# Kernel optimization log

Measured on AMD Instinct MI355X. Metric: run time of the kernel, lower is better.

The kernel has to match this reference:

```python
import jax, jax.numpy as jnp
from jax import lax
import numpy as np

# Problem dims (see init_kwargs)
B, CIN, H, W = 4, 128, 128, 128
COUT, K, STRIDE, PAD, DIL, GROUPS, OG = 128, 3, 1, 1, 1, 1, 2


def setup_inputs() -> dict:
    key = jax.random.key(0)
    k0, k1, k2 = jax.random.split(key, 3)
    x = jax.random.normal(k0, (B, CIN, H, W), dtype=jnp.float32)
    off_ch = 3 * OG * K * K  # with_mask=True -> scale=3 (dy, dx, mask)
    # Small random offset-conv weights so offsets are non-trivial (zero-init would degenerate to plain conv)
    w_off = jax.random.normal(k1, (off_ch, CIN, K, K), dtype=jnp.float32) * 0.01
    b_off = jnp.zeros((off_ch,), jnp.float32)
    stdv = 1.0 / np.sqrt(CIN * K * K)
    weight = jax.random.uniform(k2, (COUT, CIN // GROUPS, K, K), jnp.float32, -stdv, stdv)
    bias = jnp.zeros((COUT,), jnp.float32)
    return {"x": x, "w_off": w_off, "b_off": b_off, "weight": weight, "bias": bias}


def _deform_conv2d(x, offset, mask, weight, bias):
    # x: [B,C,H,W]; offset: [B,2*OG*K2,Ho,Wo]; mask: [B,OG*K2,Ho,Wo]
    Bn, C, Hn, Wn = x.shape
    O = weight.shape[0]
    K2 = K * K
    Ho = (Hn + 2 * PAD - DIL * (K - 1) - 1) // STRIDE + 1
    Wo = (Wn + 2 * PAD - DIL * (K - 1) - 1) // STRIDE + 1
    # torchvision layout: per offset group, per kernel point, (dy, dx) interleaved
    off = offset.reshape(Bn, OG, K2, 2, Ho, Wo)
    kg = (jnp.arange(K) * DIL).astype(x.dtype)
    kyf = jnp.repeat(kg, K)  # [K2] kernel row offset, k2 = i*K + j
    kxf = jnp.tile(kg, K)    # [K2] kernel col offset
    base_y = (jnp.arange(Ho) * STRIDE - PAD).astype(x.dtype)
    base_x = (jnp.arange(Wo) * STRIDE - PAD).astype(x.dtype)
    # sampling coords: [B,OG,K2,Ho,Wo]
    sy = base_y[None, None, None, :, None] + kyf[None, None, :, None, None] + off[:, :, :, 0]
    sx = base_x[None, None, None, None, :] + kxf[None, None, :, None, None] + off[:, :, :, 1]
    y0f = jnp.floor(sy)
    x0f = jnp.floor(sx)
    ly = sy - y0f  # bilinear fractional weights
    lx = sx - x0f
    y0 = y0f.astype(jnp.int32)
    x0 = x0f.astype(jnp.int32)
    Cg = C // OG
    xg = x.reshape(Bn, OG, Cg, Hn * Wn)

    def gather(iy, ix):
        # zero-padding semantics: out-of-range corners contribute 0
        valid = ((iy >= 0) & (iy < Hn) & (ix >= 0) & (ix < Wn)).astype(x.dtype)
        idx = (jnp.clip(iy, 0, Hn - 1) * Wn + jnp.clip(ix, 0, Wn - 1)).reshape(Bn, OG, 1, -1)
        v = jnp.take_along_axis(xg, idx, axis=3).reshape(Bn, OG, Cg, K2, Ho, Wo)
        return v * valid[:, :, None]

    v00 = gather(y0, x0)
    v01 = gather(y0, x0 + 1)
    v10 = gather(y0 + 1, x0)
    v11 = gather(y0 + 1, x0 + 1)
    wy = ly[:, :, None]  # broadcast over channel dim
    wx = lx[:, :, None]
    val = (v00 * (1 - wy) * (1 - wx) + v01 * (1 - wy) * wx
           + v10 * wy * (1 - wx) + v11 * wy * wx)
    # modulated DCNv2: multiply sampled values by sigmoid mask
    val = val * mask.reshape(Bn, OG, 1, K2, Ho, Wo)
    # im2col GEMM: cols [B,G,(C/G)*K2,Ho*Wo] x weight [G,O/G,(C/G)*K2]
    cols = val.reshape(Bn, GROUPS, (C // GROUPS) * K2, Ho * Wo)
    wg = weight.reshape(GROUPS, O // GROUPS, (C // GROUPS) * K2)
    out = jnp.einsum('gok,bgkn->bgon', wg, cols).reshape(Bn, O, Ho, Wo)
    return out + bias[None, :, None, None]


def reference(x, w_off, b_off, weight, bias):
    off_out = lax.conv_general_dilated(
        x, w_off, (STRIDE, STRIDE), [(PAD, PAD), (PAD, PAD)],
        rhs_dilation=(DIL, DIL), dimension_numbers=('NCHW', 'OIHW', 'NCHW')
    ) + b_off[None, :, None, None]
    oh, ow, m = jnp.split(off_out, 3, axis=1)
    offset = jnp.concatenate([oh, ow], axis=1)
    mask = jax.nn.sigmoid(m)
    return _deform_conv2d(x, offset, mask, weight, bias)
```

## Files before the change

kernel.cpp:

```cpp
#include <hip/hip_runtime.h>
#include <math.h>

#define NB 4
#define NC 128
#define NH 128
#define NW 128
#define NHW (NH*NW)
#define NCOUT 128

#define SY_OFF 0
#define SX_OFF 1179648
#define MK_OFF 2359296
#define WOFF_OFF 3538944
#define WMAIN_OFF 3580416
#define XT_OFF 3663360

typedef short short8 __attribute__((ext_vector_type(8)));
typedef float f32x4 __attribute__((ext_vector_type(4)));

__device__ inline short f2bf(float f) {
    unsigned u = __float_as_uint(f);
    u = (u + 0x7FFFu + ((u >> 16) & 1u)) >> 16;
    return (short)u;
}
__device__ inline unsigned pack2(float lo, float hi) {
    unsigned r;
    asm("v_cvt_pk_bf16_f32 %0, %1, %2" : "=v"(r) : "v"(lo), "v"(hi));
    return r;
}
__device__ inline float bflo(unsigned u) { return __uint_as_float(u << 16); }
__device__ inline float bfhi(unsigned u) { return __uint_as_float(u & 0xffff0000u); }
__device__ inline unsigned pkf16(float a, float b) {
    auto h = __builtin_amdgcn_cvt_pkrtz(a, b);
    unsigned r; __builtin_memcpy(&r, &h, 4); return r;
}
__device__ inline float f16f(unsigned s) {
    unsigned short us = (unsigned short)s;
    __fp16 h; __builtin_memcpy(&h, &us, 2); return (float)h;
}
__device__ inline void gload_lds16(const void* g, void* l) {
    __builtin_amdgcn_global_load_lds(
        (const __attribute__((address_space(1))) unsigned int*)g,
        (__attribute__((address_space(3))) unsigned int*)l, 16, 0, 0);
}

__global__ void wtrans_kernel(const float* __restrict__ w_off,
                              const float* __restrict__ weight,
                              float* __restrict__ ws)
{
    int i = blockIdx.x * 256 + threadIdx.x;
    if (i < 36*2304) {
        int s = i / 2304, rem = i - s*2304;
        int row = rem / 36, c = rem - row*36;
        int chunk = s / 9, k2 = s - 9*chunk;
        float v = (row < 54 && c < 32) ? w_off[(row*NC + chunk*32 + c)*9 + k2] : 0.f;
        ((short*)(ws + WOFF_OFF))[i] = f2bf(v);
    } else if (i < 36*2304 + 36*4608) {
        int j = i - 36*2304;
        int s = j / 4608, rem = j - s*4608;
        int row = rem / 36, c = rem - row*36;
        int chunk = s / 9, k2 = s - 9*chunk;
        float v = (c < 32) ? weight[(row*NC + chunk*32 + c)*9 + k2] : 0.f;
        ((short*)(ws + WMAIN_OFF))[j] = f2bf(v);
    }
}

__global__ __launch_bounds__(256) void xtrans_kernel(
    const float* __restrict__ x, float* __restrict__ ws)
{
    short* xT = (short*)(ws + XT_OFF);
    const int bid = blockIdx.x;
    const int ys = bid & 15, cg = (bid >> 4) & 15, b = bid >> 8;
    const int col = threadIdx.x & 127, rr = threadIdx.x >> 7;
    const float* xb = x + ((long)(b*NC + cg*8))*NHW;
#pragma unroll
    for (int yy = 0; yy < 4; ++yy) {
        const int y = ys*8 + yy*2 + rr;
        const float* p = xb + y*NW + col;
        float v[8];
#pragma unroll
        for (int q = 0; q < 8; ++q) v[q] = p[q*NHW];
        uint4 u = make_uint4(pack2(v[0],v[1]), pack2(v[2],v[3]),
                             pack2(v[4],v[5]), pack2(v[6],v[7]));
        *(uint4*)&xT[(((long)(b*16+cg)*NH + y)*NW + col)*8] = u;
    }
}

__global__ __launch_bounds__(512, 4) void offconv_kernel(
    float* __restrict__ ws, const float* __restrict__ b_off)
{
    __shared__ short wslab[2][2304];
    int bid = blockIdx.x;
    bid = (bid & 7) * 64 + (bid >> 3);
    const int b   = bid >> 7;
    const int ho  = bid & 127;
    const int tid = threadIdx.x;
    const int lane = tid & 63;
    const int wid = tid >> 6;
    const int n = lane & 15, g = lane >> 4;
    const int px = wid*16 + n;
    const short* woff = (const short*)(ws + WOFF_OFF);
    const char*  xTb  = (const char*)((const short*)(ws + XT_OFF) + (long)b*16*NHW*8);

    f32x4 acc[4];
#pragma unroll
    for (int rf = 0; rf < 4; ++rf) acc[rf] = (f32x4){0.f,0.f,0.f,0.f};

    auto DMA = [&](int it, int buf) {
        if (tid < 288) gload_lds16(woff + it*2304 + tid*8, &wslab[buf][tid*8]);
    };
    auto LOADB = [&](int it) -> short8 {
        const int chunk = it/9, k2 = it - 9*chunk;
        const int y = ho + k2/3 - 1, xc = px + (k2%3) - 1;
        short8 bf = (short8){0,0,0,0,0,0,0,0};
        if ((unsigned)y < NH && (unsigned)xc < NW)
            bf = *(const short8*)(xTb + ((long)(chunk*4 + g)*NHW + y*NW + xc)*16);
        return bf;
    };

    DMA(0, 0);
    short8 bcur = LOADB(0);
    __syncthreads();

#pragma unroll 1
    for (int it = 0; it < 36; ++it) {
        const int cur = it & 1, nxt = cur ^ 1;
        short8 bnext;
        if (it < 35) { DMA(it+1, nxt); bnext = LOADB(it+1); }
        __builtin_amdgcn_sched_barrier(0);
#pragma unroll
        for (int rf = 0; rf < 4; ++rf) {
            short8 af = *(const short8*)&wslab[cur][(rf*16 + n)*36 + 8*g];
            acc[rf] = __builtin_amdgcn_mfma_f32_16x16x32_bf16(af, bcur, acc[rf], 0,0,0);
        }
        __syncthreads();
        bcur = bnext;
    }

#pragma unroll
    for (int rf = 0; rf < 4; ++rf) {
#pragma unroll
        for (int r = 0; r < 4; ++r) {
            int cout = 16*rf + 4*g + r;
            if (cout >= 54) continue;
            float v = acc[rf][r] + b_off[cout];
            if (cout < 36) {
                int og = cout / 18, rem = cout - 18*og;
                int k2c = rem >> 1, d = cout & 1;
                float base = d ? (float)(px - 1 + (k2c % 3))
                              : (float)(ho - 1 + (k2c / 3));
                ws[(d ? SX_OFF : SY_OFF) + (((b*2+og)*9 + k2c)*NHW) + ho*NW + px] = v + base;
            } else {
                int cc = cout - 36;
                int og = cc / 9, k2c = cc - 9*og;
                ws[MK_OFF + (((b*2+og)*9 + k2c)*NHW) + ho*NW + px] = 1.f/(1.f+expf(-v));
            }
        }
    }
}

__global__ __launch_bounds__(512, 4) void deform_kernel(
    const float* __restrict__ ws_c, float* __restrict__ ws,
    const float* __restrict__ bias, float* __restrict__ out)
{
    __shared__ short4 pI[18][128];
    __shared__ uint2  pWp[18][128];
    __shared__ short  vals[2][128][40];
    __shared__ short  wslab[2][4608];

    int bid = blockIdx.x;
    bid = (bid & 7) * 64 + (bid >> 3);
    const int b   = bid >> 7;
    const int ho  = bid & 127;
    const int tid = threadIdx.x;
    const int lane = tid & 63;
    const int wid = tid >> 6;
    const int n = lane & 15, g = lane >> 4;
    const int ch  = wid & 1;
    const int pxq = wid >> 1;
    const int sp  = tid & 127;
    const int sub = tid >> 7;
    const short* wmn = (const short*)(ws + WMAIN_OFF);
    const char*  xTb = (const char*)((const short*)(ws + XT_OFF) + (long)b*16*NHW*8);

    f32x4 acc[4][2];
#pragma unroll
    for (int rf = 0; rf < 4; ++rf) {
        acc[rf][0] = (f32x4){0.f,0.f,0.f,0.f};
        acc[rf][1] = (f32x4){0.f,0.f,0.f,0.f};
    }

    auto DMA = [&](int slabIdx, int buf) {
        const short* src = wmn + slabIdx*4608;
        gload_lds16(src + tid*8, &wslab[buf][tid*8]);
        if (tid < 64) gload_lds16(src + 4096 + tid*8, &wslab[buf][4096 + tid*8]);
    };
    auto GLOAD = [&](int j, uint4* G) {
        const int chunk = j/9;
        const int row = (j/18)*9 + (j%9);
        const short4 I = pI[row][sp];
        const char* xp = xTb + (long)(chunk*4 + sub)*(NHW*16);
        G[0] = *(const uint4*)(xp + (((int)I.x) << 4));
        G[1] = *(const uint4*)(xp + (((int)I.y) << 4));
        G[2] = *(const uint4*)(xp + (((int)I.z) << 4));
        G[3] = *(const uint4*)(xp + (((int)I.w) << 4));
    };
    auto FIN = [&](int j, uint4* G, int buf) {
        const int row = (j/18)*9 + (j%9);
        const uint2 wp = *(const uint2*)&pWp[row][sp];
        const float W0 = f16f(wp.x), W1 = f16f(wp.x >> 16);
        const float W2 = f16f(wp.y), W3 = f16f(wp.y >> 16);
        uint4 u; unsigned* up = (unsigned*)&u;
        const unsigned* a = (const unsigned*)&G[0];
        const unsigned* bq = (const unsigned*)&G[1];
        const unsigned* c = (const unsigned*)&G[2];
        const unsigned* d = (const unsigned*)&G[3];
#pragma unroll
        for (int e = 0; e < 4; ++e) {
            float lo = W0*bflo(a[e]) + W1*bflo(bq[e]) + W2*bflo(c[e]) + W3*bflo(d[e]);
            float hi = W0*bfhi(a[e]) + W1*bfhi(bq[e]) + W2*bfhi(c[e]) + W3*bfhi(d[e]);
            up[e] = pack2(lo, hi);
        }
        *(uint4*)&vals[buf][sp][sub*8] = u;
    };

    DMA(0, 0);

    for (int e = tid; e < 2304; e += 512) {
        const int og = e / 1152, rem = e - og*1152;
        const int k2 = rem >> 7, px = rem & 127;
        const int sidx = (((b*2+og)*9 + k2)*NHW) + ho*NW + px;
        const float sy = ws[SY_OFF + sidx];
        const float sx = ws[SX_OFF + sidx];
        const float m  = ws[MK_OFF + sidx];
        const float y0f = floorf(sy), x0f = floorf(sx);
        const float ly = sy - y0f, lx = sx - x0f;
        const int y0 = (int)y0f, x0i = (int)x0f;
        const int y1 = y0 + 1, x1 = x0i + 1;
        const bool vy0 = (unsigned)y0 < NH, vy1 = (unsigned)y1 < NH;
        const bool vx0 = (unsigned)x0i < NW, vx1 = (unsigned)x1 < NW;
        const int cy0 = min(max(y0,0),NH-1), cy1 = min(max(y1,0),NH-1);
        const int cx0 = min(max(x0i,0),NW-1), cx1 = min(max(x1,0),NW-1);
        pI[og*9+k2][px] = make_short4(
            (short)(cy0*NW + cx0), (short)(cy0*NW + cx1),
            (short)(cy1*NW + cx0), (short)(cy1*NW + cx1));
        const float W0 = (vy0 && vx0) ? (1.f-ly)*(1.f-lx)*m : 0.f;
        const float W1 = (vy0 && vx1) ? (1.f-ly)*lx*m       : 0.f;
        const float W2 = (vy1 && vx0) ? ly*(1.f-lx)*m       : 0.f;
        const float W3 = (vy1 && vx1) ? ly*lx*m             : 0.f;
        pWp[og*9+k2][px] = make_uint2(pkf16(W0, W1), pkf16(W2, W3));
    }
    __syncthreads();

    uint4 GA[4], GB[4];
    GLOAD(0, GA);
    FIN(0, GA, 0);
    GLOAD(1, GB);
    asm volatile("s_waitcnt lgkmcnt(0)" ::: "memory");
    __builtin_amdgcn_s_barrier();
    __builtin_amdgcn_sched_barrier(0);

    auto BODY = [&](int it, uint4* Gfree, uint4* Gheld) {
        const int cur = it & 1, nxt = cur ^ 1;
        if (it < 35) DMA(it+1, nxt);
        if (it < 34) GLOAD(it+2, Gfree);
        __builtin_amdgcn_sched_barrier(0);
        {
            short8 bf0 = *(const short8*)&vals[cur][pxq*32 + n][8*g];
            short8 bf1 = *(const short8*)&vals[cur][pxq*32 + 16 + n][8*g];
#pragma unroll
            for (int rf = 0; rf < 4; ++rf) {
                short8 af = *(const short8*)&wslab[cur][(ch*64 + rf*16 + n)*36 + 8*g];
                acc[rf][0] = __builtin_amdgcn_mfma_f32_16x16x32_bf16(af, bf0, acc[rf][0], 0,0,0);
                acc[rf][1] = __builtin_amdgcn_mfma_f32_16x16x32_bf16(af, bf1, acc[rf][1], 0,0,0);
            }
        }
        __builtin_amdgcn_sched_barrier(0);
        if (it < 35) FIN(it+1, Gheld, nxt);
        if (it < 34) {
            asm volatile("s_waitcnt vmcnt(4) lgkmcnt(0)" ::: "memory");
            __builtin_amdgcn_s_barrier();
            __builtin_amdgcn_sched_barrier(0);
        } else if (it == 34) {
            asm volatile("s_waitcnt vmcnt(0) lgkmcnt(0)" ::: "memory");
            __builtin_amdgcn_s_barrier();
            __builtin_amdgcn_sched_barrier(0);
        }
    };
#pragma unroll 1
    for (int t = 0; t < 18; ++t) {
        BODY(2*t,     GA, GB);
        BODY(2*t + 1, GB, GA);
    }

#pragma unroll
    for (int rf = 0; rf < 4; ++rf) {
#pragma unroll
        for (int pxb = 0; pxb < 2; ++pxb) {
            const int px = pxq*32 + pxb*16 + n;
#pragma unroll
            for (int r = 0; r < 4; ++r) {
                const int cout = ch*64 + rf*16 + 4*g + r;
                out[((b*NCOUT + cout)*NH + ho)*NW + px] = acc[rf][pxb][r] + bias[cout];
            }
        }
    }
}

extern "C" void kernel_launch(void* const* d_in, const int* in_sizes, int n_in,
                              void* d_out, int out_size, void* d_ws, size_t ws_size,
                              hipStream_t stream)
{
    const float* x      = (const float*)d_in[0];
    const float* w_off  = (const float*)d_in[1];
    const float* b_off  = (const float*)d_in[2];
    const float* weight = (const float*)d_in[3];
    const float* bias   = (const float*)d_in[4];
    float* out = (float*)d_out;
    float* ws  = (float*)d_ws;

    hipLaunchKernelGGL(wtrans_kernel, dim3(972), dim3(256), 0, stream,
                       w_off, weight, ws);
    hipLaunchKernelGGL(xtrans_kernel, dim3(1024), dim3(256), 0, stream,
                       x, ws);
    hipLaunchKernelGGL(offconv_kernel, dim3(NB*NH), dim3(512), 0, stream,
                       ws, b_off);
    hipLaunchKernelGGL(deform_kernel, dim3(NB*NH), dim3(512), 0, stream,
                       ws, ws, bias, out);
}
```

Baseline: 92.58 us.

## Fuse offset conv into deformable conv kernel via shared-memory handoff

Merges the offset-convolution kernel and the deformable-conv kernel into one launch. Each block computes its row's offset/mask conv outputs into LDS and builds its bilinear sample tables from there, instead of writing sy/sx/mask planes to global workspace and reading them back. LDS regions are aliased so the combined kernel keeps a similar footprint. One scheduling barrier inside the main loop is also dropped. The cost is a longer per-block serial phase before the main GEMM pipeline starts, with less overlap across blocks.

```diff
diff --git a/kernel.cpp b/kernel.cpp
--- a/kernel.cpp
+++ b/kernel.cpp
@@ -8,9 +8,6 @@
 #define NHW (NH*NW)
 #define NCOUT 128
 
-#define SY_OFF 0
-#define SX_OFF 1179648
-#define MK_OFF 2359296
 #define WOFF_OFF 3538944
 #define WMAIN_OFF 3580416
 #define XT_OFF 3663360
@@ -86,10 +83,19 @@
     }
 }
 
-__global__ __launch_bounds__(512, 4) void offconv_kernel(
-    float* __restrict__ ws, const float* __restrict__ b_off)
+__global__ __launch_bounds__(512, 4) void fused_kernel(
+    const float* __restrict__ b_off, const float* __restrict__ bias,
+    float* __restrict__ ws, float* __restrict__ out)
 {
-    __shared__ short wslab[2][2304];
+    __shared__ short4 pI[18][128];
+    __shared__ uint2  pWp[18][128];
+    __shared__ char   creg[38912];
+
+    float* convout = (float*)creg;
+    short (*wsoff)[2304] = (short(*)[2304])(creg + 28512);
+    short (*vals)[128][40] = (short(*)[128][40])creg;
+    short (*wslab)[4608] = (short(*)[4608])(creg + 20480);
+
     int bid = blockIdx.x;
     bid = (bid & 7) * 64 + (bid >> 3);
     const int b   = bid >> 7;
@@ -98,90 +104,88 @@
     const int lane = tid & 63;
     const int wid = tid >> 6;
     const int n = lane & 15, g = lane >> 4;
-    const int px = wid*16 + n;
-    const short* woff = (const short*)(ws + WOFF_OFF);
-    const char*  xTb  = (const char*)((const short*)(ws + XT_OFF) + (long)b*16*NHW*8);
-
-    f32x4 acc[4];
-#pragma unroll
-    for (int rf = 0; rf < 4; ++rf) acc[rf] = (f32x4){0.f,0.f,0.f,0.f};
-
-    auto DMA = [&](int it, int buf) {
-        if (tid < 288) gload_lds16(woff + it*2304 + tid*8, &wslab[buf][tid*8]);
-    };
-    auto LOADB = [&](int it) -> short8 {
-        const int chunk = it/9, k2 = it - 9*chunk;
-        const int y = ho + k2/3 - 1, xc = px + (k2%3) - 1;
-        short8 bf = (short8){0,0,0,0,0,0,0,0};
-        if ((unsigned)y < NH && (unsigned)xc < NW)
-            bf = *(const short8*)(xTb + ((long)(chunk*4 + g)*NHW + y*NW + xc)*16);
-        return bf;
-    };
-
-    DMA(0, 0);
-    short8 bcur = LOADB(0);
-    __syncthreads();
-
-#pragma unroll 1
-    for (int it = 0; it < 36; ++it) {
-        const int cur = it & 1, nxt = cur ^ 1;
-        short8 bnext;
-        if (it < 35) { DMA(it+1, nxt); bnext = LOADB(it+1); }
-        __builtin_amdgcn_sched_barrier(0);
-#pragma unroll
-        for (int rf = 0; rf < 4; ++rf) {
-            short8 af = *(const short8*)&wslab[cur][(rf*16 + n)*36 + 8*g];
-            acc[rf] = __builtin_amdgcn_mfma_f32_16x16x32_bf16(af, bcur, acc[rf], 0,0,0);
-        }
-        __syncthreads();
-        bcur = bnext;
-    }
-
-#pragma unroll
-    for (int rf = 0; rf < 4; ++rf) {
-#pragma unroll
-        for (int r = 0; r < 4; ++r) {
-            int cout = 16*rf + 4*g + r;
-            if (cout >= 54) continue;
-            float v = acc[rf][r] + b_off[cout];
-            if (cout < 36) {
-                int og = cout / 18, rem = cout - 18*og;
-                int k2c = rem >> 1, d = cout & 1;
-                float base = d ? (float)(px - 1 + (k2c % 3))
-                              : (float)(ho - 1 + (k2c / 3));
-                ws[(d ? SX_OFF : SY_OFF) + (((b*2+og)*9 + k2c)*NHW) + ho*NW + px] = v + base;
-            } else {
-                int cc = cout - 36;
-                int og = cc / 9, k2c = cc - 9*og;
-                ws[MK_OFF + (((b*2+og)*9 + k2c)*NHW) + ho*NW + px] = 1.f/(1.f+expf(-v));
-            }
-        }
-    }
-}
-
-__global__ __launch_bounds__(512, 4) void deform_kernel(
-    const float* __restrict__ ws_c, float* __restrict__ ws,
-    const float* __restrict__ bias, float* __restrict__ out)
-{
-    __shared__ short4 pI[18][128];
-    __shared__ uint2  pWp[18][128];
-    __shared__ short  vals[2][128][40];
-    __shared__ short  wslab[2][4608];
-
-    int bid = blockIdx.x;
-    bid = (bid & 7) * 64 + (bid >> 3);
-    const int b   = bid >> 7;
-    const int ho  = bid & 127;
-    const int tid = threadIdx.x;
-    const int lane = tid & 63;
-    const int wid = tid >> 6;
-    const int n = lane & 15, g = lane >> 4;
+    const int px1 = wid*16 + n;
     const int ch  = wid & 1;
     const int pxq = wid >> 1;
     const int sp  = tid & 127;
     const int sub = tid >> 7;
-    const short* wmn = (const short*)(ws + WMAIN_OFF);
-    const char*  xTb = (const char*)((const short*)(ws + XT_OFF) + (long)b*16*NHW*8);
+    const short* woff = (const short*)(ws + WOFF_OFF);
+    const short* wmn  = (const short*)(ws + WMAIN_OFF);
+    const char*  xTb  = (const char*)((const short*)(ws + XT_OFF) + (long)b*16*NHW*8);
+
+    {
+        f32x4 accO[4];
+#pragma unroll
+        for (int rf = 0; rf < 4; ++rf) accO[rf] = (f32x4){0.f,0.f,0.f,0.f};
+
+        auto DMAo = [&](int it, int buf) {
+            if (tid < 288) gload_lds16(woff + it*2304 + tid*8, &wsoff[buf][tid*8]);
+        };
+        auto LOADB = [&](int it) -> short8 {
+            const int chunk = it/9, k2 = it - 9*chunk;
+            const int y = ho + k2/3 - 1, xc = px1 + (k2%3) - 1;
+            short8 bf = (short8){0,0,0,0,0,0,0,0};
+            if ((unsigned)y < NH && (unsigned)xc < NW)
+                bf = *(const short8*)(xTb + ((long)(chunk*4 + g)*NHW + y*NW + xc)*16);
+            return bf;
+        };
+
+        DMAo(0, 0);
+        short8 bcur = LOADB(0);
+        __syncthreads();
+
+#pragma unroll 1
+        for (int it = 0; it < 36; ++it) {
+            const int cur = it & 1, nxt = cur ^ 1;
+            short8 bnext;
+            if (it < 35) { DMAo(it+1, nxt); bnext = LOADB(it+1); }
+            __builtin_amdgcn_sched_barrier(0);
+#pragma unroll
+            for (int rf = 0; rf < 4; ++rf) {
+                short8 af = *(const short8*)&wsoff[cur][(rf*16 + n)*36 + 8*g];
+                accO[rf] = __builtin_amdgcn_mfma_f32_16x16x32_bf16(af, bcur, accO[rf], 0,0,0);
+            }
+            __syncthreads();
+            bcur = bnext;
+        }
+
+#pragma unroll
+        for (int rf = 0; rf < 4; ++rf) {
+#pragma unroll
+            for (int r = 0; r < 4; ++r) {
+                const int cout = 16*rf + 4*g + r;
+                if (cout < 54) convout[cout*132 + px1] = accO[rf][r];
+            }
+        }
+    }
+    __syncthreads();
+
+    for (int e = tid; e < 2304; e += 512) {
+        const int og = e / 1152, rem = e - og*1152;
+        const int k2 = rem >> 7, px = rem & 127;
+        const int c_sy = og*18 + 2*k2, c_sx = c_sy + 1, c_m = 36 + og*9 + k2;
+        const float sy = convout[c_sy*132 + px] + b_off[c_sy] + (float)(ho - 1 + k2/3);
+        const float sx = convout[c_sx*132 + px] + b_off[c_sx] + (float)(px - 1 + k2%3);
+        const float mr = convout[c_m*132 + px] + b_off[c_m];
+        const float m  = 1.f / (1.f + expf(-mr));
+        const float y0f = floorf(sy), x0f = floorf(sx);
+        const float ly = sy - y0f, lx = sx - x0f;
+        const int y0 = (int)y0f, x0i = (int)x0f;
+        const int y1 = y0 + 1, x1 = x0i + 1;
+        const bool vy0 = (unsigned)y0 < NH, vy1 = (unsigned)y1 < NH;
+        const bool vx0 = (unsigned)x0i < NW, vx1 = (unsigned)x1 < NW;
+        const int cy0 = min(max(y0,0),NH-1), cy1 = min(max(y1,0),NH-1);
+        const int cx0 = min(max(x0i,0),NW-1), cx1 = min(max(x1,0),NW-1);
+        pI[og*9+k2][px] = make_short4(
+            (short)(cy0*NW + cx0), (short)(cy0*NW + cx1),
+            (short)(cy1*NW + cx0), (short)(cy1*NW + cx1));
+        const float W0 = (vy0 && vx0) ? (1.f-ly)*(1.f-lx)*m : 0.f;
+        const float W1 = (vy0 && vx1) ? (1.f-ly)*lx*m       : 0.f;
+        const float W2 = (vy1 && vx0) ? ly*(1.f-lx)*m       : 0.f;
+        const float W3 = (vy1 && vx1) ? ly*lx*m             : 0.f;
+        pWp[og*9+k2][px] = make_uint2(pkf16(W0, W1), pkf16(W2, W3));
+    }
+    __syncthreads();
 
     f32x4 acc[4][2];
 #pragma unroll
@@ -190,7 +194,7 @@
         acc[rf][1] = (f32x4){0.f,0.f,0.f,0.f};
     }
 
-    auto DMA = [&](int slabIdx, int buf) {
+    auto DMAm = [&](int slabIdx, int buf) {
         const short* src = wmn + slabIdx*4608;
         gload_lds16(src + tid*8, &wslab[buf][tid*8]);
         if (tid < 64) gload_lds16(src + 4096 + tid*8, &wslab[buf][4096 + tid*8]);
@@ -224,35 +228,8 @@
         *(uint4*)&vals[buf][sp][sub*8] = u;
     };
 
-    DMA(0, 0);
-
-    for (int e = tid; e < 2304; e += 512) {
-        const int og = e / 1152, rem = e - og*1152;
-        const int k2 = rem >> 7, px = rem & 127;
-        const int sidx = (((b*2+og)*9 + k2)*NHW) + ho*NW + px;
-        const float sy = ws[SY_OFF + sidx];
-        const float sx = ws[SX_OFF + sidx];
-        const float m  = ws[MK_OFF + sidx];
-        const float y0f = floorf(sy), x0f = floorf(sx);
-        const float ly = sy - y0f, lx = sx - x0f;
-        const int y0 = (int)y0f, x0i = (int)x0f;
-        const int y1 = y0 + 1, x1 = x0i + 1;
-        const bool vy0 = (unsigned)y0 < NH, vy1 = (unsigned)y1 < NH;
-        const bool vx0 = (unsigned)x0i < NW, vx1 = (unsigned)x1 < NW;
-        const int cy0 = min(max(y0,0),NH-1), cy1 = min(max(y1,0),NH-1);
-        const int cx0 = min(max(x0i,0),NW-1), cx1 = min(max(x1,0),NW-1);
-        pI[og*9+k2][px] = make_short4(
-            (short)(cy0*NW + cx0), (short)(cy0*NW + cx1),
-            (short)(cy1*NW + cx0), (short)(cy1*NW + cx1));
-        const float W0 = (vy0 && vx0) ? (1.f-ly)*(1.f-lx)*m : 0.f;
-        const float W1 = (vy0 && vx1) ? (1.f-ly)*lx*m       : 0.f;
-        const float W2 = (vy1 && vx0) ? ly*(1.f-lx)*m       : 0.f;
-        const float W3 = (vy1 && vx1) ? ly*lx*m             : 0.f;
-        pWp[og*9+k2][px] = make_uint2(pkf16(W0, W1), pkf16(W2, W3));
-    }
-    __syncthreads();
-
     uint4 GA[4], GB[4];
+    DMAm(0, 0);
     GLOAD(0, GA);
     FIN(0, GA, 0);
     GLOAD(1, GB);
@@ -262,7 +239,7 @@
 
     auto BODY = [&](int it, uint4* Gfree, uint4* Gheld) {
         const int cur = it & 1, nxt = cur ^ 1;
-        if (it < 35) DMA(it+1, nxt);
+        if (it < 35) DMAm(it+1, nxt);
         if (it < 34) GLOAD(it+2, Gfree);
         __builtin_amdgcn_sched_barrier(0);
         {
@@ -275,7 +252,6 @@
                 acc[rf][1] = __builtin_amdgcn_mfma_f32_16x16x32_bf16(af, bf1, acc[rf][1], 0,0,0);
             }
         }
-        __builtin_amdgcn_sched_barrier(0);
         if (it < 35) FIN(it+1, Gheld, nxt);
         if (it < 34) {
             asm volatile("s_waitcnt vmcnt(4) lgkmcnt(0)" ::: "memory");
@@ -323,8 +299,6 @@
                        w_off, weight, ws);
     hipLaunchKernelGGL(xtrans_kernel, dim3(1024), dim3(256), 0, stream,
                        x, ws);
-    hipLaunchKernelGGL(offconv_kernel, dim3(NB*NH), dim3(512), 0, stream,
-                       ws, b_off);
-    hipLaunchKernelGGL(deform_kernel, dim3(NB*NH), dim3(512), 0, stream,
-                       ws, ws, bias, out);
-}
+    hipLaunchKernelGGL(fused_kernel, dim3(NB*NH), dim3(512), 0, stream,
+                       b_off, bias, ws, out);
+}
```

Measured after the change: 177.0 us. +91.1%, slower.

## Keep sampled columns in registers as MFMA A operand, split rows into half-row blocks

Applied to the files above, without the earlier changes.

The deformable conv kernel now launches twice as many 256-thread blocks, each covering half an output row (64 pixels). Each wave samples its own 16 pixels across 32 channels and feeds the bilinear result straight into the MFMA A operand from registers. This drops the vals LDS staging buffer and its write/read traffic. Each wave computes all 128 output channels, so weight slabs are read from LDS by every wave, and the output is written as float4 stores. The trade-off is more per-block setup and weight DMA per output pixel, in exchange for less LDS use and no intermediate LDS round trip.

```diff
diff --git a/kernel.cpp b/kernel.cpp
--- a/kernel.cpp
+++ b/kernel.cpp
@@ -159,77 +159,76 @@
     }
 }
 
-__global__ __launch_bounds__(512, 4) void deform_kernel(
+__global__ __launch_bounds__(256, 4) void deform_kernel(
     const float* __restrict__ ws_c, float* __restrict__ ws,
     const float* __restrict__ bias, float* __restrict__ out)
 {
-    __shared__ short4 pI[18][128];
-    __shared__ uint2  pWp[18][128];
-    __shared__ short  vals[2][128][40];
+    __shared__ short4 pI[18][64];
+    __shared__ uint2  pWp[18][64];
     __shared__ short  wslab[2][4608];
 
     int bid = blockIdx.x;
-    bid = (bid & 7) * 64 + (bid >> 3);
-    const int b   = bid >> 7;
-    const int ho  = bid & 127;
+    bid = (bid & 7) * 128 + (bid >> 3);
+    const int b   = bid >> 8;
+    const int ho  = (bid >> 1) & 127;
+    const int wb  = (bid & 1) * 64;
     const int tid = threadIdx.x;
     const int lane = tid & 63;
     const int wid = tid >> 6;
     const int n = lane & 15, g = lane >> 4;
-    const int ch  = wid & 1;
-    const int pxq = wid >> 1;
-    const int sp  = tid & 127;
-    const int sub = tid >> 7;
+    const int pxl = 16*wid + n;
     const short* wmn = (const short*)(ws + WMAIN_OFF);
     const char*  xTb = (const char*)((const short*)(ws + XT_OFF) + (long)b*16*NHW*8);
 
-    f32x4 acc[4][2];
-#pragma unroll
-    for (int rf = 0; rf < 4; ++rf) {
-        acc[rf][0] = (f32x4){0.f,0.f,0.f,0.f};
-        acc[rf][1] = (f32x4){0.f,0.f,0.f,0.f};
-    }
+    f32x4 acc[8];
+#pragma unroll
+    for (int rf = 0; rf < 8; ++rf) acc[rf] = (f32x4){0.f,0.f,0.f,0.f};
 
     auto DMA = [&](int slabIdx, int buf) {
         const short* src = wmn + slabIdx*4608;
         gload_lds16(src + tid*8, &wslab[buf][tid*8]);
+        gload_lds16(src + 2048 + tid*8, &wslab[buf][2048 + tid*8]);
         if (tid < 64) gload_lds16(src + 4096 + tid*8, &wslab[buf][4096 + tid*8]);
     };
-    auto GLOAD = [&](int j, uint4* G) {
-        const int chunk = j/9;
-        const int row = (j/18)*9 + (j%9);
-        const short4 I = pI[row][sp];
-        const char* xp = xTb + (long)(chunk*4 + sub)*(NHW*16);
-        G[0] = *(const uint4*)(xp + (((int)I.x) << 4));
-        G[1] = *(const uint4*)(xp + (((int)I.y) << 4));
-        G[2] = *(const uint4*)(xp + (((int)I.z) << 4));
-        G[3] = *(const uint4*)(xp + (((int)I.w) << 4));
-    };
-    auto FIN = [&](int j, uint4* G, int buf) {
-        const int row = (j/18)*9 + (j%9);
-        const uint2 wp = *(const uint2*)&pWp[row][sp];
-        const float W0 = f16f(wp.x), W1 = f16f(wp.x >> 16);
-        const float W2 = f16f(wp.y), W3 = f16f(wp.y >> 16);
-        uint4 u; unsigned* up = (unsigned*)&u;
-        const unsigned* a = (const unsigned*)&G[0];
-        const unsigned* bq = (const unsigned*)&G[1];
-        const unsigned* c = (const unsigned*)&G[2];
-        const unsigned* d = (const unsigned*)&G[3];
-#pragma unroll
-        for (int e = 0; e < 4; ++e) {
-            float lo = W0*bflo(a[e]) + W1*bflo(bq[e]) + W2*bflo(c[e]) + W3*bflo(d[e]);
-            float hi = W0*bfhi(a[e]) + W1*bfhi(bq[e]) + W2*bfhi(c[e]) + W3*bfhi(d[e]);
-            up[e] = pack2(lo, hi);
-        }
-        *(uint4*)&vals[buf][sp][sub*8] = u;
-    };
+
+#define GLOAD(j, G0, G1, G2, G3) do {                                   \
+        const int row_ = ((j)/18)*9 + (j)%9;                            \
+        const int chunk_ = (j)/9;                                       \
+        const short4 I_ = pI[row_][pxl];                                \
+        const char* xp_ = xTb + (long)(chunk_*4 + g)*(NHW*16);          \
+        G0 = *(const uint4*)(xp_ + (((int)I_.x) << 4));                 \
+        G1 = *(const uint4*)(xp_ + (((int)I_.y) << 4));                 \
+        G2 = *(const uint4*)(xp_ + (((int)I_.z) << 4));                 \
+        G3 = *(const uint4*)(xp_ + (((int)I_.w) << 4));                 \
+    } while (0)
+
+#define FIN(j, G0, G1, G2, G3, Adst) do {                               \
+        const int row_ = ((j)/18)*9 + (j)%9;                            \
+        const uint2 wp_ = *(const uint2*)&pWp[row_][pxl];               \
+        const float W0_ = f16f(wp_.x), W1_ = f16f(wp_.x >> 16);         \
+        const float W2_ = f16f(wp_.y), W3_ = f16f(wp_.y >> 16);         \
+        uint4 u_; unsigned* up_ = (unsigned*)&u_;                       \
+        const unsigned* a_ = (const unsigned*)&G0;                      \
+        const unsigned* b_ = (const unsigned*)&G1;                      \
+        const unsigned* c_ = (const unsigned*)&G2;                      \
+        const unsigned* d_ = (const unsigned*)&G3;                      \
+        _Pragma("unroll")                                               \
+        for (int e = 0; e < 4; ++e) {                                   \
+            float lo = W0_*bflo(a_[e]) + W1_*bflo(b_[e])                \
+                     + W2_*bflo(c_[e]) + W3_*bflo(d_[e]);               \
+            float hi = W0_*bfhi(a_[e]) + W1_*bfhi(b_[e])                \
+                     + W2_*bfhi(c_[e]) + W3_*bfhi(d_[e]);               \
+            up_[e] = pack2(lo, hi);                                     \
+        }                                                               \
+        __builtin_memcpy(&Adst, &u_, 16);                               \
+    } while (0)
 
     DMA(0, 0);
 
-    for (int e = tid; e < 2304; e += 512) {
-        const int og = e / 1152, rem = e - og*1152;
-        const int k2 = rem >> 7, px = rem & 127;
-        const int sidx = (((b*2+og)*9 + k2)*NHW) + ho*NW + px;
+    for (int e = tid; e < 1152; e += 256) {
+        const int row = e >> 6, p = e & 63;
+        const int og = row / 9, k2 = row - 9*og;
+        const int sidx = (((b*2+og)*9 + k2)*NHW) + ho*NW + wb + p;
         const float sy = ws[SY_OFF + sidx];
         const float sx = ws[SX_OFF + sidx];
         const float m  = ws[MK_OFF + sidx];
@@ -241,69 +240,61 @@
         const bool vx0 = (unsigned)x0i < NW, vx1 = (unsigned)x1 < NW;
         const int cy0 = min(max(y0,0),NH-1), cy1 = min(max(y1,0),NH-1);
         const int cx0 = min(max(x0i,0),NW-1), cx1 = min(max(x1,0),NW-1);
-        pI[og*9+k2][px] = make_short4(
+        pI[row][p] = make_short4(
             (short)(cy0*NW + cx0), (short)(cy0*NW + cx1),
             (short)(cy1*NW + cx0), (short)(cy1*NW + cx1));
         const float W0 = (vy0 && vx0) ? (1.f-ly)*(1.f-lx)*m : 0.f;
         const float W1 = (vy0 && vx1) ? (1.f-ly)*lx*m       : 0.f;
         const float W2 = (vy1 && vx0) ? ly*(1.f-lx)*m       : 0.f;
         const float W3 = (vy1 && vx1) ? ly*lx*m             : 0.f;
-        pWp[og*9+k2][px] = make_uint2(pkf16(W0, W1), pkf16(W2, W3));
+        pWp[row][p] = make_uint2(pkf16(W0, W1), pkf16(W2, W3));
     }
     __syncthreads();
 
-    uint4 GA[4], GB[4];
-    GLOAD(0, GA);
-    FIN(0, GA, 0);
-    GLOAD(1, GB);
-    asm volatile("s_waitcnt lgkmcnt(0)" ::: "memory");
-    __builtin_amdgcn_s_barrier();
-    __builtin_amdgcn_sched_barrier(0);
-
-    auto BODY = [&](int it, uint4* Gfree, uint4* Gheld) {
-        const int cur = it & 1, nxt = cur ^ 1;
-        if (it < 35) DMA(it+1, nxt);
-        if (it < 34) GLOAD(it+2, Gfree);
-        __builtin_amdgcn_sched_barrier(0);
-        {
-            short8 bf0 = *(const short8*)&vals[cur][pxq*32 + n][8*g];
-            short8 bf1 = *(const short8*)&vals[cur][pxq*32 + 16 + n][8*g];
-#pragma unroll
-            for (int rf = 0; rf < 4; ++rf) {
-                short8 af = *(const short8*)&wslab[cur][(ch*64 + rf*16 + n)*36 + 8*g];
-                acc[rf][0] = __builtin_amdgcn_mfma_f32_16x16x32_bf16(af, bf0, acc[rf][0], 0,0,0);
-                acc[rf][1] = __builtin_amdgcn_mfma_f32_16x16x32_bf16(af, bf1, acc[rf][1], 0,0,0);
-            }
-        }
-        __builtin_amdgcn_sched_barrier(0);
-        if (it < 35) FIN(it+1, Gheld, nxt);
-        if (it < 34) {
-            asm volatile("s_waitcnt vmcnt(4) lgkmcnt(0)" ::: "memory");
-            __builtin_amdgcn_s_barrier();
-            __builtin_amdgcn_sched_barrier(0);
-        } else if (it == 34) {
-            asm volatile("s_waitcnt vmcnt(0) lgkmcnt(0)" ::: "memory");
-            __builtin_amdgcn_s_barrier();
-            __builtin_amdgcn_sched_barrier(0);
-        }
-    };
+    uint4 Ga0, Ga1, Ga2, Ga3, Gb0, Gb1, Gb2, Gb3;
+    short8 Acur, Anxt;
+    GLOAD(0, Ga0, Ga1, Ga2, Ga3);
+    FIN(0, Ga0, Ga1, Ga2, Ga3, Acur);
+    GLOAD(1, Gb0, Gb1, Gb2, Gb3);
+
+#define BODY(it, Ain, Aout, H0, H1, H2, H3, F0, F1, F2, F3) do {        \
+        const int cur_ = (it) & 1, nxt_ = cur_ ^ 1;                     \
+        if ((it) < 35) DMA((it)+1, nxt_);                               \
+        if ((it) < 34) GLOAD((it)+2, F0, F1, F2, F3);                   \
+        __builtin_amdgcn_sched_barrier(0);                              \
+        _Pragma("unroll")                                               \
+        for (int rf = 0; rf < 8; ++rf) {                                \
+            short8 bf = *(const short8*)&wslab[cur_][(16*rf + n)*36 + 8*g]; \
+            acc[rf] = __builtin_amdgcn_mfma_f32_16x16x32_bf16(Ain, bf, acc[rf], 0,0,0); \
+        }                                                               \
+        if ((it) < 35) FIN((it)+1, H0, H1, H2, H3, Aout);               \
+        if ((it) < 34) {                                                \
+            asm volatile("s_waitcnt vmcnt(4) lgkmcnt(0)" ::: "memory"); \
+            __builtin_amdgcn_s_barrier();                               \
+            __builtin_amdgcn_sched_barrier(0);                          \
+        } else if ((it) == 34) {                                        \
+            asm volatile("s_waitcnt vmcnt(0) lgkmcnt(0)" ::: "memory"); \
+            __builtin_amdgcn_s_barrier();                               \
+            __builtin_amdgcn_sched_barrier(0);                          \
+        }                                                               \
+    } while (0)
+
 #pragma unroll 1
     for (int t = 0; t < 18; ++t) {
-        BODY(2*t,     GA, GB);
-        BODY(2*t + 1, GB, GA);
-    }
-
-#pragma unroll
-    for (int rf = 0; rf < 4; ++rf) {
-#pragma unroll
-        for (int pxb = 0; pxb < 2; ++pxb) {
-            const int px = pxq*32 + pxb*16 + n;
-#pragma unroll
-            for (int r = 0; r < 4; ++r) {
-                const int cout = ch*64 + rf*16 + 4*g + r;
-                out[((b*NCOUT + cout)*NH + ho)*NW + px] = acc[rf][pxb][r] + bias[cout];
-            }
-        }
+        BODY(2*t,     Acur, Anxt, Gb0, Gb1, Gb2, Gb3, Ga0, Ga1, Ga2, Ga3);
+        BODY(2*t + 1, Anxt, Acur, Ga0, Ga1, Ga2, Ga3, Gb0, Gb1, Gb2, Gb3);
+    }
+#undef BODY
+#undef GLOAD
+#undef FIN
+
+#pragma unroll
+    for (int rf = 0; rf < 8; ++rf) {
+        const int cout = 16*rf + n;
+        const float bb = bias[cout];
+        float4 o = make_float4(acc[rf][0]+bb, acc[rf][1]+bb,
+                               acc[rf][2]+bb, acc[rf][3]+bb);
+        *(float4*)&out[((b*NCOUT + cout)*NH + ho)*NW + wb + 16*wid + 4*g] = o;
     }
 }
 
@@ -325,6 +316,6 @@
                        x, ws);
     hipLaunchKernelGGL(offconv_kernel, dim3(NB*NH), dim3(512), 0, stream,
                        ws, b_off);
-    hipLaunchKernelGGL(deform_kernel, dim3(NB*NH), dim3(512), 0, stream,
+    hipLaunchKernelGGL(deform_kernel, dim3(NB*NH*2), dim3(256), 0, stream,
                        ws, ws, bias, out);
 }
```

After: 99.80 us. 7.8% more time.
